# Kernel optimization log

Measured on AMD Instinct MI355X. Metric: run time of the kernel, lower is better.

Reference implementation:

```python
import jax, jax.numpy as jnp
import numpy as np

DIM = 768
NUM_HEADS = 12
HEAD_DIM = DIM // NUM_HEADS
SCALE = HEAD_DIM ** -0.5


def setup_inputs() -> dict:
    key = jax.random.key(0)
    ks = jax.random.split(key, 8)
    B, Nx, Ny = 4, 1024, 2048
    std = DIM ** -0.5
    return {
        "x": jax.random.normal(ks[0], (B, Nx, DIM), dtype=jnp.float32),
        "y": jax.random.normal(ks[1], (B, Ny, DIM), dtype=jnp.float32),
        "Wq": jax.random.normal(ks[2], (DIM, DIM), dtype=jnp.float32) * std,
        "Wk": jax.random.normal(ks[3], (DIM, DIM), dtype=jnp.float32) * std,
        "Wv": jax.random.normal(ks[4], (DIM, DIM), dtype=jnp.float32) * std,
        "Wproj": jax.random.normal(ks[5], (DIM, DIM), dtype=jnp.float32) * std,
        "bproj": jnp.zeros((DIM,), dtype=jnp.float32),
    }


def reference(x, y, Wq, Wk, Wv, Wproj, bproj):
    B, Nx, C = x.shape
    Ny = y.shape[1]
    H, D = NUM_HEADS, HEAD_DIM
    # Linear projections (torch nn.Linear: x @ W.T), then split heads -> [B,H,N,D]
    q = (x @ Wq.T).reshape(B, Nx, H, D).transpose(0, 2, 1, 3)
    k = (y @ Wk.T).reshape(B, Ny, H, D).transpose(0, 2, 1, 3)
    v = (y @ Wv.T).reshape(B, Ny, H, D).transpose(0, 2, 1, 3)
    # Manual attention: full [B,H,Nx,Ny] score matrix (faithful to source)
    attn = jnp.einsum("bhqd,bhkd->bhqk", q, k) * SCALE
    attn = jax.nn.softmax(attn, axis=-1)
    out = jnp.einsum("bhqk,bhkd->bhqd", attn, v)
    out = out.transpose(0, 2, 1, 3).reshape(B, Nx, C)
    return out @ Wproj.T + bproj
```

## Files before the change

kernel.cpp:

```cpp
#include <hip/hip_runtime.h>
#include <hip/hip_bf16.h>

typedef unsigned short u16;
typedef __attribute__((ext_vector_type(8))) short bf16x8;
typedef __attribute__((ext_vector_type(4))) float f32x4;
typedef __attribute__((ext_vector_type(16))) float f32x16;
typedef __attribute__((ext_vector_type(4))) unsigned u32x4;

#define MFMA(a, b, c) __builtin_amdgcn_mfma_f32_16x16x32_bf16(a, b, c, 0, 0, 0)
#define MFMA32(a, b, c) __builtin_amdgcn_mfma_f32_32x32x16_bf16(a, b, c, 0, 0, 0)

#define STAGE16(g, l) __builtin_amdgcn_global_load_lds( \
    (const __attribute__((address_space(1))) void*)(g),  \
    (__attribute__((address_space(3))) void*)(l), 16, 0, 0)

#define EXP2(x) __builtin_amdgcn_exp2f(x)

__device__ __forceinline__ u16 f2bf(float f) {
  union { float f; unsigned u; } v; v.f = f;
  return (u16)((v.u + 0x7fffu + ((v.u >> 16) & 1u)) >> 16);
}

__device__ __forceinline__ unsigned pack_bf2(float lo, float hi) {
  unsigned r;
  asm("v_cvt_pk_bf16_f32 %0, %1, %2" : "=v"(r) : "v"(lo), "v"(hi));
  return r;
}

__device__ __forceinline__ void pl32swap(unsigned &a, unsigned &b) {
  asm("v_permlane32_swap_b32 %0, %1" : "+v"(a), "+v"(b));
}

__global__ __launch_bounds__(256) void convert_all(
    const float* __restrict__ x, const float* __restrict__ y,
    const float* __restrict__ wq, const float* __restrict__ wk,
    const float* __restrict__ wv, const float* __restrict__ wp,
    u16* __restrict__ xb, u16* __restrict__ yb,
    u16* __restrict__ wqb, u16* __restrict__ wkb,
    u16* __restrict__ wvb, u16* __restrict__ wpb)
{
  constexpr int G0 = 4096 * 768 / 4;
  constexpr int G1 = G0 + 8192 * 768 / 4;
  constexpr int GW = 768 * 768 / 4;
  int g = blockIdx.x * 256 + threadIdx.x;
  const float* s; u16* d; int o;
  if      (g < G0)          { s = x;  d = xb;  o = g; }
  else if (g < G1)          { s = y;  d = yb;  o = g - G0; }
  else if (g < G1 + GW)     { s = wq; d = wqb; o = g - G1; }
  else if (g < G1 + 2*GW)   { s = wk; d = wkb; o = g - G1 - GW; }
  else if (g < G1 + 3*GW)   { s = wv; d = wvb; o = g - G1 - 2*GW; }
  else if (g < G1 + 4*GW)   { s = wp; d = wpb; o = g - G1 - 3*GW; }
  else return;
  float4 v = reinterpret_cast<const float4*>(s)[o];
  ushort4 r;
  r.x = f2bf(v.x); r.y = f2bf(v.y); r.z = f2bf(v.z); r.w = f2bf(v.w);
  reinterpret_cast<ushort4*>(d)[o] = r;
}

template <bool PROJ>
__global__ __launch_bounds__(256) void gemm_k(
    const u16* __restrict__ A0, const u16* __restrict__ A1,
    const u16* __restrict__ W0, const u16* __restrict__ W1,
    const u16* __restrict__ W2,
    u16* __restrict__ Qa, u16* __restrict__ Ka, u16* __restrict__ Vw,
    const float* __restrict__ bias, float* __restrict__ fout)
{
  __shared__ u16 sA[2][128 * 64];
  __shared__ u16 sB[2][128 * 64];

  const int nper = PROJ ? 24 : 120;
  int bid = (blockIdx.x & 7) * nper + (blockIdx.x >> 3);

  const u16 *A, *W;
  int mode, mt, nt;
  if (PROJ)           { mode = 3; A = A0; W = W0; mt = bid / 6;        nt = bid % 6; }
  else if (bid < 192) { mode = 0; A = A0; W = W0; mt = bid / 6;        nt = bid % 6; }
  else if (bid < 576) { mode = 1; A = A1; W = W1; mt = (bid-192) / 6;  nt = (bid-192) % 6; }
  else                { mode = 2; A = A1; W = W2; mt = (bid-576) / 6;  nt = (bid-576) % 6; }

  const int tid = threadIdx.x;
  const int w = tid >> 6, l = tid & 63;
  const int wm = w >> 1, wn = w & 1;
  const int g = l >> 4, m = l & 15;

  const int mbase = mt * 128, nbase = nt * 128;

  const int srow = l >> 3;
  const int schunk = ((l & 7) ^ srow) * 8;
  const u16* Ag = A + (size_t)(mbase + srow) * 768 + schunk;
  const u16* Wg = W + (size_t)(nbase + srow) * 768 + schunk;

  f32x4 acc[4][4] = {};

#pragma unroll
  for (int i = 0; i < 4; ++i) {
    const int ri = (i * 4 + w) * 8;
    STAGE16(Ag + (size_t)ri * 768, (char*)sA[0] + ri * 128);
    STAGE16(Wg + (size_t)ri * 768, (char*)sB[0] + ri * 128);
  }

  for (int kt = 0; kt < 12; ++kt) {
    __syncthreads();

    if (kt < 11) {
      const int ko = (kt + 1) * 64;
      const int nb = (kt + 1) & 1;
#pragma unroll
      for (int i = 0; i < 4; ++i) {
        const int ri = (i * 4 + w) * 8;
        STAGE16(Ag + (size_t)ri * 768 + ko, (char*)sA[nb] + ri * 128);
        STAGE16(Wg + (size_t)ri * 768 + ko, (char*)sB[nb] + ri * 128);
      }
    }

    const int cb = kt & 1;
    bf16x8 af[2][4], bfr[2][4];
#pragma unroll
    for (int c = 0; c < 2; ++c)
#pragma unroll
      for (int t = 0; t < 4; ++t) {
        const int ar = wm * 64 + t * 16 + m;
        const int br = wn * 64 + t * 16 + m;
        const int cp = ((c * 4 + g) ^ (l & 7)) * 16;
        af[c][t]  = *reinterpret_cast<const bf16x8*>((const char*)sA[cb] + ar * 128 + cp);
        bfr[c][t] = *reinterpret_cast<const bf16x8*>((const char*)sB[cb] + br * 128 + cp);
      }
#pragma unroll
    for (int c = 0; c < 2; ++c)
#pragma unroll
      for (int mi = 0; mi < 4; ++mi)
#pragma unroll
        for (int ni = 0; ni < 4; ++ni)
          acc[mi][ni] = MFMA(af[c][mi], bfr[c][ni], acc[mi][ni]);
  }

  const float QSCALE = 0.18033688011112042f;
  const int rowb = mbase + wm * 64 + g * 4;
  const int colb = nbase + wn * 64 + m;
#pragma unroll
  for (int mi = 0; mi < 4; ++mi) {
#pragma unroll
    for (int ni = 0; ni < 4; ++ni) {
      const int col = colb + ni * 16;
      const int h = col >> 6, d = col & 63;
      const int t_ = d >> 4, hh = (d >> 3) & 1, di = d & 7;
      const int fo = t_ * 512 + hh * 256 + di;
      if constexpr (PROJ) {
#pragma unroll
        for (int r = 0; r < 4; ++r) {
          const int row = rowb + mi * 16 + r;
          fout[(size_t)row * 768 + col] = acc[mi][ni][r] + bias[col];
        }
      } else {
        if (mode == 0) {
#pragma unroll
          for (int r = 0; r < 4; ++r) {
            const int row = rowb + mi * 16 + r;
            const int b_ = row >> 10, n = row & 1023;
            Qa[((size_t)(b_ * 12 + h) * 32 + (n >> 5)) * 2048 + fo + (n & 31) * 8] =
                f2bf(acc[mi][ni][r] * QSCALE);
          }
        } else if (mode == 1) {
#pragma unroll
          for (int r = 0; r < 4; ++r) {
            const int row = rowb + mi * 16 + r;
            const int b_ = row >> 11, n = row & 2047;
            Ka[(size_t)(b_ * 12 + h) * 131072 + (n >> 5) * 2048 + fo + (n & 31) * 8] =
                f2bf(acc[mi][ni][r]);
          }
        } else {
          const int row = rowb + mi * 16;
          const int b_ = row >> 11, n = row & 2047;
          ushort4 pk;
          pk.x = f2bf(acc[mi][ni][0]); pk.y = f2bf(acc[mi][ni][1]);
          pk.z = f2bf(acc[mi][ni][2]); pk.w = f2bf(acc[mi][ni][3]);
          *reinterpret_cast<ushort4*>(
              Vw + (size_t)(b_ * 12 + h) * 131072 + (n >> 3) * 512 + d * 8 + (n & 7)) = pk;
        }
      }
    }
  }
}

__global__ __launch_bounds__(128, 3) void attn_fwd(
    const u16* __restrict__ Qa, const u16* __restrict__ Ka,
    const u16* __restrict__ Vw, u16* __restrict__ AOb)
{
  __shared__ float cO[32 * 64];
  __shared__ float cL[32];

  const int bid = blockIdx.x;
  const int bh = bid % 48, qt = bid / 48;
  const int tid = threadIdx.x;
  const int w = tid >> 6, l = tid & 63;
  const int h = l >> 5, q = l & 31;

  const u16* qb = Qa + (size_t)(bh * 32 + qt) * 2048 + h * 256 + q * 8;
  bf16x8 qf[4];
#pragma unroll
  for (int t = 0; t < 4; ++t)
    qf[t] = *reinterpret_cast<const bf16x8*>(qb + t * 512);

  const u16* kb = Ka + (size_t)bh * 131072 + (size_t)w * 65536 + h * 256 + q * 8;
  const u16* vb = Vw + (size_t)bh * 131072 + (size_t)w * 65536 + h * 512 + q * 8;

  bf16x8 ones;
#pragma unroll
  for (int i = 0; i < 8; ++i) ones[i] = (short)0x3F80;

  f32x16 o0 = {}, o1 = {}, la = {};

  for (int kt = 0; kt < 16; ++kt) {
    const u16* kp = kb + kt * 4096;
    const u16* vp = vb + kt * 4096;

    bf16x8 kf0[4], kf1[4];
#pragma unroll
    for (int t = 0; t < 4; ++t) {
      kf0[t] = *reinterpret_cast<const bf16x8*>(kp + t * 512);
      kf1[t] = *reinterpret_cast<const bf16x8*>(kp + 2048 + t * 512);
    }

    f32x16 s0 = {}, s1 = {};
    __builtin_amdgcn_s_setprio(1);
#pragma unroll
    for (int t = 0; t < 4; ++t) {
      s0 = MFMA32(kf0[t], qf[t], s0);
      s1 = MFMA32(kf1[t], qf[t], s1);
    }
    __builtin_amdgcn_s_setprio(0);

    bf16x8 vf0[4], vf1[4];
#pragma unroll
    for (int t = 0; t < 4; ++t) {
      vf0[t] = *reinterpret_cast<const bf16x8*>(vp + t * 1024);
      vf1[t] = *reinterpret_cast<const bf16x8*>(vp + t * 1024 + 256);
    }

    float p0[16], p1[16];
#pragma unroll
    for (int r = 0; r < 16; ++r) p0[r] = EXP2(s0[r]);
#pragma unroll
    for (int r = 0; r < 16; ++r) p1[r] = EXP2(s1[r]);

    unsigned pk[2][4][2];
#pragma unroll
    for (int qd = 0; qd < 4; ++qd) {
      pk[0][qd][0] = pack_bf2(p0[4*qd+0], p0[4*qd+1]);
      pk[0][qd][1] = pack_bf2(p0[4*qd+2], p0[4*qd+3]);
      pk[1][qd][0] = pack_bf2(p1[4*qd+0], p1[4*qd+1]);
      pk[1][qd][1] = pack_bf2(p1[4*qd+2], p1[4*qd+3]);
    }

    __builtin_amdgcn_s_setprio(1);
#pragma unroll
    for (int t = 0; t < 4; ++t) {
      const int c = t >> 1, j0 = 2 * (t & 1);
      unsigned x0 = pk[c][j0][0], y0 = pk[c][j0 + 1][0];
      unsigned x1 = pk[c][j0][1], y1 = pk[c][j0 + 1][1];
      pl32swap(x0, y0);
      pl32swap(x1, y1);
      u32x4 fv; fv[0] = x0; fv[1] = x1; fv[2] = y0; fv[3] = y1;
      const bf16x8 af = __builtin_bit_cast(bf16x8, fv);
      o0 = MFMA32(af, vf0[t], o0);
      o1 = MFMA32(af, vf1[t], o1);
      la = MFMA32(af, ones, la);
    }
    __builtin_amdgcn_s_setprio(0);
  }

  if (w == 1) {
#pragma unroll
    for (int r = 0; r < 16; ++r) {
      const int crow = (r >> 2) * 8 + 4 * h + (r & 3);
      cO[crow * 64 + q]      = o0[r];
      cO[crow * 64 + 32 + q] = o1[r];
      if (q == 0) cL[crow] = la[r];
    }
  }
  __syncthreads();
  if (w == 0) {
    const int b_ = bh / 12, hd = bh % 12;
#pragma unroll
    for (int r = 0; r < 16; ++r) {
      const int crow = (r >> 2) * 8 + 4 * h + (r & 3);
      const float lt = la[r] + cL[crow];
      const float rl = 1.f / lt;
      const float ot0 = o0[r] + cO[crow * 64 + q];
      const float ot1 = o1[r] + cO[crow * 64 + 32 + q];
      u16* dst = AOb + ((size_t)b_ * 1024 + qt * 32 + crow) * 768 + hd * 64 + q;
      dst[0]  = f2bf(ot0 * rl);
      dst[32] = f2bf(ot1 * rl);
    }
  }
}

extern "C" void kernel_launch(void* const* d_in, const int* in_sizes, int n_in,
                              void* d_out, int out_size, void* d_ws, size_t ws_size,
                              hipStream_t stream)
{
  const float* x  = (const float*)d_in[0];
  const float* y  = (const float*)d_in[1];
  const float* wq = (const float*)d_in[2];
  const float* wk = (const float*)d_in[3];
  const float* wv = (const float*)d_in[4];
  const float* wp = (const float*)d_in[5];
  const float* bp = (const float*)d_in[6];
  float* out = (float*)d_out;

  char* ws = (char*)d_ws;
  u16* xb  = (u16*)ws; ws += (size_t)4096 * 768 * 2;
  u16* yb  = (u16*)ws; ws += (size_t)8192 * 768 * 2;
  u16* wqb = (u16*)ws; ws += (size_t)768 * 768 * 2;
  u16* wkb = (u16*)ws; ws += (size_t)768 * 768 * 2;
  u16* wvb = (u16*)ws; ws += (size_t)768 * 768 * 2;
  u16* wpb = (u16*)ws; ws += (size_t)768 * 768 * 2;
  u16* Qa  = (u16*)ws; ws += (size_t)4096 * 768 * 2;
  u16* Ka  = (u16*)ws; ws += (size_t)8192 * 768 * 2;
  u16* Vw  = (u16*)ws; ws += (size_t)8192 * 768 * 2;
  u16* AOb = (u16*)ws; ws += (size_t)4096 * 768 * 2;

  convert_all<<<11520, 256, 0, stream>>>(x, y, wq, wk, wv, wp,
                                         xb, yb, wqb, wkb, wvb, wpb);
  gemm_k<false><<<960, 256, 0, stream>>>(xb, yb, wqb, wkb, wvb,
                                         Qa, Ka, Vw, nullptr, nullptr);
  attn_fwd<<<1536, 128, 0, stream>>>(Qa, Ka, Vw, AOb);
  gemm_k<true><<<192, 256, 0, stream>>>(AOb, nullptr, wpb, nullptr, nullptr,
                                        nullptr, nullptr, nullptr, bp, out);
}
```

Before: 101.9 us.

## Split attention KV range across two blocks and combine partials in separate kernel

The attention kernel now launches twice as many blocks, and each block covers half of the key/value sequence, so each wave processes a quarter instead of a half. Unnormalized fp32 partial outputs and row sums are written to workspace, and a new combine kernel adds the two halves, normalizes and converts to bf16. The aim is more parallelism and occupancy on the GPU's compute units, paid for with an extra kernel launch and roughly 25 MB of fp32 partial traffic. The split relies on the kernel's existing softmax with no max subtraction, which is why plain sums can be combined.

Result: slower. 111.5 us (+9.5%).

```diff
diff --git a/kernel.cpp b/kernel.cpp
--- a/kernel.cpp
+++ b/kernel.cpp
@@ -184,13 +184,16 @@
 
 __global__ __launch_bounds__(128, 3) void attn_fwd(
     const u16* __restrict__ Qa, const u16* __restrict__ Ka,
-    const u16* __restrict__ Vw, u16* __restrict__ AOb)
+    const u16* __restrict__ Vw, float* __restrict__ Opart,
+    float* __restrict__ Lpart)
 {
   __shared__ float cO[32 * 64];
   __shared__ float cL[32];
 
   const int bid = blockIdx.x;
-  const int bh = bid % 48, qt = bid / 48;
+  const int bh = bid % 48;
+  const int qt = (bid / 48) % 32;
+  const int half = bid / 1536;
   const int tid = threadIdx.x;
   const int w = tid >> 6, l = tid & 63;
   const int h = l >> 5, q = l & 31;
@@ -201,8 +204,9 @@
   for (int t = 0; t < 4; ++t)
     qf[t] = *reinterpret_cast<const bf16x8*>(qb + t * 512);
 
-  const u16* kb = Ka + (size_t)bh * 131072 + (size_t)w * 65536 + h * 256 + q * 8;
-  const u16* vb = Vw + (size_t)bh * 131072 + (size_t)w * 65536 + h * 512 + q * 8;
+  const int quarter = half * 2 + w;
+  const u16* kb = Ka + (size_t)bh * 131072 + (size_t)quarter * 32768 + h * 256 + q * 8;
+  const u16* vb = Vw + (size_t)bh * 131072 + (size_t)quarter * 32768 + h * 512 + q * 8;
 
   bf16x8 ones;
 #pragma unroll
@@ -210,7 +214,7 @@
 
   f32x16 o0 = {}, o1 = {}, la = {};
 
-  for (int kt = 0; kt < 16; ++kt) {
+  for (int kt = 0; kt < 8; ++kt) {
     const u16* kp = kb + kt * 4096;
     const u16* vp = vb + kt * 4096;
 
@@ -280,19 +284,37 @@
   }
   __syncthreads();
   if (w == 0) {
-    const int b_ = bh / 12, hd = bh % 12;
+    float* Op = Opart + ((size_t)(half * 48 + bh) * 1024 + qt * 32) * 64;
+    float* Lp = Lpart + (size_t)(half * 48 + bh) * 1024 + qt * 32;
 #pragma unroll
     for (int r = 0; r < 16; ++r) {
       const int crow = (r >> 2) * 8 + 4 * h + (r & 3);
-      const float lt = la[r] + cL[crow];
-      const float rl = 1.f / lt;
-      const float ot0 = o0[r] + cO[crow * 64 + q];
-      const float ot1 = o1[r] + cO[crow * 64 + 32 + q];
-      u16* dst = AOb + ((size_t)b_ * 1024 + qt * 32 + crow) * 768 + hd * 64 + q;
-      dst[0]  = f2bf(ot0 * rl);
-      dst[32] = f2bf(ot1 * rl);
-    }
-  }
+      Op[crow * 64 + q]      = o0[r] + cO[crow * 64 + q];
+      Op[crow * 64 + 32 + q] = o1[r] + cO[crow * 64 + 32 + q];
+      if (q == 0) Lp[crow] = la[r] + cL[crow];
+    }
+  }
+}
+
+__global__ __launch_bounds__(256) void combine(
+    const float* __restrict__ Opart, const float* __restrict__ Lpart,
+    u16* __restrict__ AOb)
+{
+  const int id = blockIdx.x * 256 + threadIdx.x;
+  const int d4 = id & 15;
+  const int bn = id >> 4;
+  const float4* O0 = reinterpret_cast<const float4*>(Opart);
+  const float4 a = O0[(size_t)bn * 16 + d4];
+  const float4 b = O0[(size_t)(49152 + bn) * 16 + d4];
+  const float rl = 1.f / (Lpart[bn] + Lpart[49152 + bn]);
+  ushort4 r;
+  r.x = f2bf((a.x + b.x) * rl);
+  r.y = f2bf((a.y + b.y) * rl);
+  r.z = f2bf((a.z + b.z) * rl);
+  r.w = f2bf((a.w + b.w) * rl);
+  const int bh = bn >> 10, n = bn & 1023;
+  *reinterpret_cast<ushort4*>(
+      AOb + ((size_t)(bh / 12) * 1024 + n) * 768 + (bh % 12) * 64 + d4 * 4) = r;
 }
 
 extern "C" void kernel_launch(void* const* d_in, const int* in_sizes, int n_in,
@@ -319,12 +341,15 @@
   u16* Ka  = (u16*)ws; ws += (size_t)8192 * 768 * 2;
   u16* Vw  = (u16*)ws; ws += (size_t)8192 * 768 * 2;
   u16* AOb = (u16*)ws; ws += (size_t)4096 * 768 * 2;
+  float* Opart = (float*)ws; ws += (size_t)2 * 48 * 1024 * 64 * 4;
+  float* Lpart = (float*)ws; ws += (size_t)2 * 48 * 1024 * 4;
 
   convert_all<<<11520, 256, 0, stream>>>(x, y, wq, wk, wv, wp,
                                          xb, yb, wqb, wkb, wvb, wpb);
   gemm_k<false><<<960, 256, 0, stream>>>(xb, yb, wqb, wkb, wvb,
                                          Qa, Ka, Vw, nullptr, nullptr);
-  attn_fwd<<<1536, 128, 0, stream>>>(Qa, Ka, Vw, AOb);
+  attn_fwd<<<3072, 128, 0, stream>>>(Qa, Ka, Vw, Opart, Lpart);
+  combine<<<3072, 256, 0, stream>>>(Opart, Lpart, AOb);
   gemm_k<true><<<192, 256, 0, stream>>>(AOb, nullptr, wpb, nullptr, nullptr,
                                         nullptr, nullptr, nullptr, bp, out);
 }
```

## Compute softmax row sums in VALU and unroll key loop by two

Applied to the files above, without the earlier changes.

Drops the extra MFMA against a ones vector that accumulated softmax denominators. Each lane now sums its exp values with adds plus a cross-half shuffle and keeps a running scalar, which the two waves combine through shared memory. The key loop is manually unrolled to handle two key tiles per iteration, issuing K loads for both tiles up front and the second V tile's loads inside the body to hide memory latency. This raises register pressure, and the denominator is now summed from fp32 values rather than the bf16-rounded ones used for the numerator.

Result: no change. 103.6 us (+1.7%).

```diff
diff --git a/kernel.cpp b/kernel.cpp
--- a/kernel.cpp
+++ b/kernel.cpp
@@ -187,7 +187,7 @@
     const u16* __restrict__ Vw, u16* __restrict__ AOb)
 {
   __shared__ float cO[32 * 64];
-  __shared__ float cL[32];
+  __shared__ float cL[2][32];
 
   const int bid = blockIdx.x;
   const int bh = bid % 48, qt = bid / 48;
@@ -204,79 +204,147 @@
   const u16* kb = Ka + (size_t)bh * 131072 + (size_t)w * 65536 + h * 256 + q * 8;
   const u16* vb = Vw + (size_t)bh * 131072 + (size_t)w * 65536 + h * 512 + q * 8;
 
-  bf16x8 ones;
-#pragma unroll
-  for (int i = 0; i < 8; ++i) ones[i] = (short)0x3F80;
-
-  f32x16 o0 = {}, o1 = {}, la = {};
-
-  for (int kt = 0; kt < 16; ++kt) {
-    const u16* kp = kb + kt * 4096;
-    const u16* vp = vb + kt * 4096;
-
-    bf16x8 kf0[4], kf1[4];
+  f32x16 o0 = {}, o1 = {};
+  float lrun = 0.f;
+
+#pragma unroll 1
+  for (int kt2 = 0; kt2 < 8; ++kt2) {
+    const u16* kpa = kb + (size_t)kt2 * 8192;
+    const u16* vpa = vb + (size_t)kt2 * 8192;
+
+    bf16x8 kfa0[4], kfa1[4], kfb0[4], kfb1[4], vfa0[4], vfa1[4];
 #pragma unroll
     for (int t = 0; t < 4; ++t) {
-      kf0[t] = *reinterpret_cast<const bf16x8*>(kp + t * 512);
-      kf1[t] = *reinterpret_cast<const bf16x8*>(kp + 2048 + t * 512);
-    }
-
-    f32x16 s0 = {}, s1 = {};
-    __builtin_amdgcn_s_setprio(1);
+      kfa0[t] = *reinterpret_cast<const bf16x8*>(kpa + t * 512);
+      kfa1[t] = *reinterpret_cast<const bf16x8*>(kpa + 2048 + t * 512);
+    }
 #pragma unroll
     for (int t = 0; t < 4; ++t) {
-      s0 = MFMA32(kf0[t], qf[t], s0);
-      s1 = MFMA32(kf1[t], qf[t], s1);
-    }
-    __builtin_amdgcn_s_setprio(0);
-
-    bf16x8 vf0[4], vf1[4];
+      kfb0[t] = *reinterpret_cast<const bf16x8*>(kpa + 4096 + t * 512);
+      kfb1[t] = *reinterpret_cast<const bf16x8*>(kpa + 6144 + t * 512);
+    }
 #pragma unroll
     for (int t = 0; t < 4; ++t) {
-      vf0[t] = *reinterpret_cast<const bf16x8*>(vp + t * 1024);
-      vf1[t] = *reinterpret_cast<const bf16x8*>(vp + t * 1024 + 256);
-    }
-
-    float p0[16], p1[16];
-#pragma unroll
-    for (int r = 0; r < 16; ++r) p0[r] = EXP2(s0[r]);
-#pragma unroll
-    for (int r = 0; r < 16; ++r) p1[r] = EXP2(s1[r]);
-
-    unsigned pk[2][4][2];
-#pragma unroll
-    for (int qd = 0; qd < 4; ++qd) {
-      pk[0][qd][0] = pack_bf2(p0[4*qd+0], p0[4*qd+1]);
-      pk[0][qd][1] = pack_bf2(p0[4*qd+2], p0[4*qd+3]);
-      pk[1][qd][0] = pack_bf2(p1[4*qd+0], p1[4*qd+1]);
-      pk[1][qd][1] = pack_bf2(p1[4*qd+2], p1[4*qd+3]);
-    }
-
-    __builtin_amdgcn_s_setprio(1);
-#pragma unroll
-    for (int t = 0; t < 4; ++t) {
-      const int c = t >> 1, j0 = 2 * (t & 1);
-      unsigned x0 = pk[c][j0][0], y0 = pk[c][j0 + 1][0];
-      unsigned x1 = pk[c][j0][1], y1 = pk[c][j0 + 1][1];
-      pl32swap(x0, y0);
-      pl32swap(x1, y1);
-      u32x4 fv; fv[0] = x0; fv[1] = x1; fv[2] = y0; fv[3] = y1;
-      const bf16x8 af = __builtin_bit_cast(bf16x8, fv);
-      o0 = MFMA32(af, vf0[t], o0);
-      o1 = MFMA32(af, vf1[t], o1);
-      la = MFMA32(af, ones, la);
-    }
-    __builtin_amdgcn_s_setprio(0);
+      vfa0[t] = *reinterpret_cast<const bf16x8*>(vpa + t * 1024);
+      vfa1[t] = *reinterpret_cast<const bf16x8*>(vpa + t * 1024 + 256);
+    }
+
+    {
+      f32x16 s0 = {}, s1 = {};
+      __builtin_amdgcn_s_setprio(1);
+#pragma unroll
+      for (int t = 0; t < 4; ++t) {
+        s0 = MFMA32(kfa0[t], qf[t], s0);
+        s1 = MFMA32(kfa1[t], qf[t], s1);
+      }
+      __builtin_amdgcn_s_setprio(0);
+
+      float p0[16], p1[16];
+#pragma unroll
+      for (int r = 0; r < 16; ++r) p0[r] = EXP2(s0[r]);
+#pragma unroll
+      for (int r = 0; r < 16; ++r) p1[r] = EXP2(s1[r]);
+
+      float a8[8];
+#pragma unroll
+      for (int i = 0; i < 8; ++i)
+        a8[i] = (p0[2*i] + p0[2*i+1]) + (p1[2*i] + p1[2*i+1]);
+      float ts = ((a8[0]+a8[1]) + (a8[2]+a8[3])) + ((a8[4]+a8[5]) + (a8[6]+a8[7]));
+      ts += __shfl_xor(ts, 32);
+      lrun += ts;
+
+      unsigned pk[2][4][2];
+#pragma unroll
+      for (int qd = 0; qd < 4; ++qd) {
+        pk[0][qd][0] = pack_bf2(p0[4*qd+0], p0[4*qd+1]);
+        pk[0][qd][1] = pack_bf2(p0[4*qd+2], p0[4*qd+3]);
+        pk[1][qd][0] = pack_bf2(p1[4*qd+0], p1[4*qd+1]);
+        pk[1][qd][1] = pack_bf2(p1[4*qd+2], p1[4*qd+3]);
+      }
+
+      __builtin_amdgcn_s_setprio(1);
+#pragma unroll
+      for (int t = 0; t < 4; ++t) {
+        const int c = t >> 1, j0 = 2 * (t & 1);
+        unsigned x0 = pk[c][j0][0], y0 = pk[c][j0 + 1][0];
+        unsigned x1 = pk[c][j0][1], y1 = pk[c][j0 + 1][1];
+        pl32swap(x0, y0);
+        pl32swap(x1, y1);
+        u32x4 fv; fv[0] = x0; fv[1] = x1; fv[2] = y0; fv[3] = y1;
+        const bf16x8 af = __builtin_bit_cast(bf16x8, fv);
+        o0 = MFMA32(af, vfa0[t], o0);
+        o1 = MFMA32(af, vfa1[t], o1);
+      }
+      __builtin_amdgcn_s_setprio(0);
+    }
+
+    {
+      bf16x8 vfb0[4], vfb1[4];
+#pragma unroll
+      for (int t = 0; t < 4; ++t) {
+        vfb0[t] = *reinterpret_cast<const bf16x8*>(vpa + 4096 + t * 1024);
+        vfb1[t] = *reinterpret_cast<const bf16x8*>(vpa + 4096 + t * 1024 + 256);
+      }
+
+      f32x16 s0 = {}, s1 = {};
+      __builtin_amdgcn_s_setprio(1);
+#pragma unroll
+      for (int t = 0; t < 4; ++t) {
+        s0 = MFMA32(kfb0[t], qf[t], s0);
+        s1 = MFMA32(kfb1[t], qf[t], s1);
+      }
+      __builtin_amdgcn_s_setprio(0);
+
+      float p0[16], p1[16];
+#pragma unroll
+      for (int r = 0; r < 16; ++r) p0[r] = EXP2(s0[r]);
+#pragma unroll
+      for (int r = 0; r < 16; ++r) p1[r] = EXP2(s1[r]);
+
+      float a8[8];
+#pragma unroll
+      for (int i = 0; i < 8; ++i)
+        a8[i] = (p0[2*i] + p0[2*i+1]) + (p1[2*i] + p1[2*i+1]);
+      float ts = ((a8[0]+a8[1]) + (a8[2]+a8[3])) + ((a8[4]+a8[5]) + (a8[6]+a8[7]));
+      ts += __shfl_xor(ts, 32);
+      lrun += ts;
+
+      unsigned pk[2][4][2];
+#pragma unroll
+      for (int qd = 0; qd < 4; ++qd) {
+        pk[0][qd][0] = pack_bf2(p0[4*qd+0], p0[4*qd+1]);
+        pk[0][qd][1] = pack_bf2(p0[4*qd+2], p0[4*qd+3]);
+        pk[1][qd][0] = pack_bf2(p1[4*qd+0], p1[4*qd+1]);
+        pk[1][qd][1] = pack_bf2(p1[4*qd+2], p1[4*qd+3]);
+      }
+
+      __builtin_amdgcn_s_setprio(1);
+#pragma unroll
+      for (int t = 0; t < 4; ++t) {
+        const int c = t >> 1, j0 = 2 * (t & 1);
+        unsigned x0 = pk[c][j0][0], y0 = pk[c][j0 + 1][0];
+        unsigned x1 = pk[c][j0][1], y1 = pk[c][j0 + 1][1];
+        pl32swap(x0, y0);
+        pl32swap(x1, y1);
+        u32x4 fv; fv[0] = x0; fv[1] = x1; fv[2] = y0; fv[3] = y1;
+        const bf16x8 af = __builtin_bit_cast(bf16x8, fv);
+        o0 = MFMA32(af, vfb0[t], o0);
+        o1 = MFMA32(af, vfb1[t], o1);
+      }
+      __builtin_amdgcn_s_setprio(0);
+    }
   }
 
   if (w == 1) {
+    if (h == 0) cL[1][q] = lrun;
 #pragma unroll
     for (int r = 0; r < 16; ++r) {
       const int crow = (r >> 2) * 8 + 4 * h + (r & 3);
       cO[crow * 64 + q]      = o0[r];
       cO[crow * 64 + 32 + q] = o1[r];
-      if (q == 0) cL[crow] = la[r];
-    }
+    }
+  } else {
+    if (h == 0) cL[0][q] = lrun;
   }
   __syncthreads();
   if (w == 0) {
@@ -284,7 +352,7 @@
 #pragma unroll
     for (int r = 0; r < 16; ++r) {
       const int crow = (r >> 2) * 8 + 4 * h + (r & 3);
-      const float lt = la[r] + cL[crow];
+      const float lt = cL[0][crow] + cL[1][crow];
       const float rl = 1.f / lt;
       const float ot0 = o0[r] + cO[crow * 64 + q];
       const float ot1 = o1[r] + cO[crow * 64 + 32 + q];
```
